# Optimization experiments

Measured on AMD Instinct MI355X. Metric: run time of the kernel, lower is better.

Reference implementation:

```python
import jax, jax.numpy as jnp
import numpy as np


def setup_inputs() -> dict:
    key = jax.random.key(0)
    ks = jax.random.split(key, 8)
    B, T, D, H, E = 4, 1024, 1024, 4096, 8
    s = 0.02
    return {
        "x": jax.random.normal(ks[0], (B, T, D), jnp.float32),
        "gate_w": jax.random.normal(ks[1], (E, D), jnp.float32) * s,
        "router_scale": jnp.ones((1,), jnp.float32),
        "w1": jax.random.normal(ks[2], (E, H, D), jnp.float32) * s,
        "b1": jnp.zeros((E, H), jnp.float32),
        "w2": jax.random.normal(ks[3], (E, H, D), jnp.float32) * s,
        "b2": jnp.zeros((E, H), jnp.float32),
        "w3": jax.random.normal(ks[4], (E, D, H), jnp.float32) * s,
        "b3": jnp.zeros((E, D), jnp.float32),
        "top_k": 2,
    }


def reference(x, gate_w, router_scale, w1, b1, w2, b2, w3, b3, top_k):
    B, T, C = x.shape
    E = gate_w.shape[0]
    xf = x.reshape(B * T, C)                     # (N, C)
    # Router: top-k over scaled gate logits, softmax over the k selected logits
    logits = (xf @ gate_w.T) * router_scale      # (N, E)
    vals, idx = jax.lax.top_k(logits, top_k)     # (N, K)
    rw = jax.nn.softmax(vals, axis=-1)           # (N, K)
    # combine[n, e] = sum_k rw[n,k] * [idx[n,k] == e]  -- per-token expert weight
    combine = jnp.sum(jax.nn.one_hot(idx, E, dtype=xf.dtype) * rw[..., None], axis=1)  # (N, E)
    y = jnp.zeros_like(xf)
    for e in range(E):  # fixed small expert count; each iter is a dense SwiGLU
        h = jax.nn.silu(xf @ w1[e].T + b1[e]) * (xf @ w2[e].T + b2[e])  # (N, H)
        out = h @ w3[e].T + b3[e]                                        # (N, C)
        y = y + out * combine[:, e:e + 1]
    return y.reshape(B, T, C)
```

## Files before the change

### kernel.cpp

```cpp
#include <hip/hip_runtime.h>
#include <hip/hip_bf16.h>

#define NTOK 4096
#define DDIM 1024
#define HDIM 4096
#define NEXP 8
#define TM 128
#define TN 128
#define BK 64
#define LDP 72

typedef __attribute__((ext_vector_type(4))) float f32x4;
typedef __attribute__((ext_vector_type(8))) short bf16x8;
typedef __attribute__((ext_vector_type(4))) short bf16x4;

static __device__ __forceinline__ short f2bf(float f) {
  union { __hip_bfloat16 b; short s; } u;
  u.b = __float2bfloat16(f);
  return u.s;
}

static __device__ __forceinline__ void gl16(const void* g, void* l) {
  __builtin_amdgcn_global_load_lds((const __attribute__((address_space(1))) void*)g,
                                   (__attribute__((address_space(3))) void*)l, 16, 0, 0);
}

__global__ __launch_bounds__(256) void router_kernel(
    const float* __restrict__ x, const float* __restrict__ gw,
    const float* __restrict__ rs,
    int* __restrict__ tok_id, float* __restrict__ tok_w,
    int* __restrict__ counts, short* __restrict__ xb)
{
  const int wv = threadIdx.x >> 6;
  const int lane = threadIdx.x & 63;
  const int tok = blockIdx.x * 4 + wv;
  const f32x4* xr = (const f32x4*)(x + (size_t)tok * DDIM);
  f32x4 xv[4];
#pragma unroll
  for (int j = 0; j < 4; ++j) xv[j] = xr[j * 64 + lane];
  if (xb) {
#pragma unroll
    for (int j = 0; j < 4; ++j) {
      bf16x4 bv = { f2bf(xv[j][0]), f2bf(xv[j][1]), f2bf(xv[j][2]), f2bf(xv[j][3]) };
      *(bf16x4*)(xb + (size_t)tok * DDIM + (size_t)(j * 64 + lane) * 4) = bv;
    }
  }
  float lg[NEXP];
#pragma unroll
  for (int e = 0; e < NEXP; ++e) {
    const f32x4* gr = (const f32x4*)(gw + (size_t)e * DDIM);
    float s = 0.f;
#pragma unroll
    for (int j = 0; j < 4; ++j) {
      f32x4 g = gr[j * 64 + lane];
      s += g[0]*xv[j][0] + g[1]*xv[j][1] + g[2]*xv[j][2] + g[3]*xv[j][3];
    }
#pragma unroll
    for (int off = 32; off > 0; off >>= 1) s += __shfl_down(s, off, 64);
    lg[e] = s;
  }
  if (lane == 0) {
    const float scale = rs[0];
#pragma unroll
    for (int e = 0; e < NEXP; ++e) lg[e] *= scale;
    int i0 = 0;
#pragma unroll
    for (int e = 1; e < NEXP; ++e) if (lg[e] > lg[i0]) i0 = e;
    int i1 = (i0 == 0) ? 1 : 0;
#pragma unroll
    for (int e = 0; e < NEXP; ++e) if (e != i0 && lg[e] > lg[i1]) i1 = e;
    const float v0 = lg[i0], v1 = lg[i1];
    const float w0 = 1.f / (1.f + expf(v1 - v0));
    const float w1v = 1.f - w0;
    int s0 = atomicAdd(&counts[i0], 1);
    tok_id[i0 * NTOK + s0] = tok;
    tok_w[i0 * NTOK + s0] = w0;
    int s1 = atomicAdd(&counts[i1], 1);
    tok_id[i1 * NTOK + s1] = tok;
    tok_w[i1 * NTOK + s1] = w1v;
  }
}

__global__ void finalize_kernel(const int* __restrict__ counts, int* __restrict__ hoff) {
  if (threadIdx.x == 0) {
    int off = 0;
    for (int e = 0; e < NEXP; ++e) { hoff[e] = off; off += ((counts[e] + TM - 1) / TM) * TM; }
  }
}

__global__ __launch_bounds__(256) void convert_kernel(
    const float* __restrict__ src, short* __restrict__ dst, int n4)
{
  int i = blockIdx.x * 256 + threadIdx.x;
  const int stride = gridDim.x * 256;
  for (; i < n4; i += stride) {
    const f32x4 v = ((const f32x4*)src)[i];
    bf16x4 b = { f2bf(v[0]), f2bf(v[1]), f2bf(v[2]), f2bf(v[3]) };
    ((bf16x4*)dst)[i] = b;
  }
}

__global__ __launch_bounds__(256, 2) void stagea_fast(
    const short* __restrict__ xb,
    const short* __restrict__ w1b, const short* __restrict__ w2b,
    const float* __restrict__ b1, const float* __restrict__ b2,
    const int* __restrict__ tok_id,
    const int* __restrict__ counts, const int* __restrict__ hoff,
    short* __restrict__ h)
{
  const int e = blockIdx.z;
  const int cnt = counts[e];
  const int mt = blockIdx.y;
  if (mt * TM >= cnt) return;
  const int nt = blockIdx.x;

  __shared__ __align__(16) short sA[TM * BK];
  __shared__ __align__(16) short sB1[TN * BK];
  __shared__ __align__(16) short sB2[TN * BK];
  __shared__ int srow[TM];

  const int t = threadIdx.x;
  const int lane = t & 63;
  const int wv = t >> 6;

  if (t < TM) {
    int id = tok_id[e * NTOK + mt * TM + t];
    srow[t] = id < 0 ? 0 : id;
  }
  __syncthreads();

  const int sub = lane >> 3;
  const int c8  = lane & 7;
  const short* wbase1 = w1b + (size_t)e * HDIM * DDIM + (size_t)(nt * TN) * DDIM;
  const short* wbase2 = w2b + (size_t)e * HDIM * DDIM + (size_t)(nt * TN) * DDIM;
  const short* ap[4]; const short* bp1[4]; const short* bp2[4];
#pragma unroll
  for (int j = 0; j < 4; ++j) {
    const int r = wv * 32 + j * 8 + sub;
    ap[j]  = xb + (size_t)srow[r] * DDIM + c8 * 8;
    bp1[j] = wbase1 + (size_t)r * DDIM + c8 * 8;
    bp2[j] = wbase2 + (size_t)r * DDIM + c8 * 8;
  }

  const int wm = (wv >> 1) * 64;
  const int wn = (wv & 1) * 64;
  const int lr = lane & 15;
  const int lq = lane >> 4;

  f32x4 acc1[4][4] = {};
  f32x4 acc2[4][4] = {};

  for (int k0 = 0; k0 < DDIM; k0 += BK) {
#pragma unroll
    for (int j = 0; j < 4; ++j) {
      gl16(ap[j] + k0,  sA  + (wv * 4 + j) * 512);
      gl16(bp1[j] + k0, sB1 + (wv * 4 + j) * 512);
      gl16(bp2[j] + k0, sB2 + (wv * 4 + j) * 512);
    }
    __syncthreads();
#pragma unroll
    for (int ks = 0; ks < BK; ks += 32) {
      bf16x8 af[4], ba[4], bb[4];
#pragma unroll
      for (int mi = 0; mi < 4; ++mi)
        af[mi] = *(const bf16x8*)(sA + (wm + mi * 16 + lr) * BK + ks + lq * 8);
#pragma unroll
      for (int ni = 0; ni < 4; ++ni) {
        ba[ni] = *(const bf16x8*)(sB1 + (wn + ni * 16 + lr) * BK + ks + lq * 8);
        bb[ni] = *(const bf16x8*)(sB2 + (wn + ni * 16 + lr) * BK + ks + lq * 8);
      }
#pragma unroll
      for (int mi = 0; mi < 4; ++mi)
#pragma unroll
        for (int ni = 0; ni < 4; ++ni) {
          acc1[mi][ni] = __builtin_amdgcn_mfma_f32_16x16x32_bf16(af[mi], ba[ni], acc1[mi][ni], 0, 0, 0);
          acc2[mi][ni] = __builtin_amdgcn_mfma_f32_16x16x32_bf16(af[mi], bb[ni], acc2[mi][ni], 0, 0, 0);
        }
    }
    __syncthreads();
  }

  const int hbase = hoff[e] + mt * TM;
#pragma unroll
  for (int ni = 0; ni < 4; ++ni) {
    const int col = nt * TN + wn + ni * 16 + lr;
    const float bb1 = b1[e * HDIM + col];
    const float bb2 = b2[e * HDIM + col];
#pragma unroll
    for (int mi = 0; mi < 4; ++mi) {
#pragma unroll
      for (int r = 0; r < 4; ++r) {
        const int row = wm + mi * 16 + lq * 4 + r;
        const float z1 = acc1[mi][ni][r] + bb1;
        const float z2 = acc2[mi][ni][r] + bb2;
        const float hv = (z1 / (1.f + expf(-z1))) * z2;
        h[(size_t)(hbase + row) * HDIM + col] = f2bf(hv);
      }
    }
  }
}

__global__ __launch_bounds__(256, 2) void stageb_fast(
    const short* __restrict__ hm, const short* __restrict__ w3b,
    const float* __restrict__ b3,
    const int* __restrict__ tok_id, const float* __restrict__ tok_w,
    const int* __restrict__ counts, const int* __restrict__ hoff,
    float* __restrict__ y)
{
  const int e = blockIdx.z;
  const int cnt = counts[e];
  const int mt = blockIdx.y;
  if (mt * TM >= cnt) return;
  const int nt = blockIdx.x & 7;
  const int kh = blockIdx.x >> 3;

  __shared__ __align__(16) short sA[TM * BK];
  __shared__ __align__(16) short sB[TN * BK];

  const int t = threadIdx.x;
  const int lane = t & 63;
  const int wv = t >> 6;
  const int sub = lane >> 3;
  const int c8  = lane & 7;

  const short* hrow = hm + (size_t)(hoff[e] + mt * TM) * HDIM;
  const short* wbase = w3b + (size_t)e * DDIM * HDIM + (size_t)(nt * TN) * HDIM;
  const short* ap[4]; const short* bp[4];
#pragma unroll
  for (int j = 0; j < 4; ++j) {
    const int r = wv * 32 + j * 8 + sub;
    ap[j] = hrow + (size_t)r * HDIM + c8 * 8;
    bp[j] = wbase + (size_t)r * HDIM + c8 * 8;
  }

  const int wm = (wv >> 1) * 64;
  const int wn = (wv & 1) * 64;
  const int lr = lane & 15;
  const int lq = lane >> 4;

  f32x4 acc[4][4] = {};

  const int kbeg = kh * (HDIM / 2);
  for (int k0 = kbeg; k0 < kbeg + HDIM / 2; k0 += BK) {
#pragma unroll
    for (int j = 0; j < 4; ++j) {
      gl16(ap[j] + k0, sA + (wv * 4 + j) * 512);
      gl16(bp[j] + k0, sB + (wv * 4 + j) * 512);
    }
    __syncthreads();
#pragma unroll
    for (int ks = 0; ks < BK; ks += 32) {
      bf16x8 af[4], bfr[4];
#pragma unroll
      for (int mi = 0; mi < 4; ++mi)
        af[mi] = *(const bf16x8*)(sA + (wm + mi * 16 + lr) * BK + ks + lq * 8);
#pragma unroll
      for (int ni = 0; ni < 4; ++ni)
        bfr[ni] = *(const bf16x8*)(sB + (wn + ni * 16 + lr) * BK + ks + lq * 8);
#pragma unroll
      for (int mi = 0; mi < 4; ++mi)
#pragma unroll
        for (int ni = 0; ni < 4; ++ni)
          acc[mi][ni] = __builtin_amdgcn_mfma_f32_16x16x32_bf16(af[mi], bfr[ni], acc[mi][ni], 0, 0, 0);
    }
    __syncthreads();
  }

#pragma unroll
  for (int ni = 0; ni < 4; ++ni) {
    const int col = nt * TN + wn + ni * 16 + lr;
    const float bb3 = (kh == 0) ? b3[e * DDIM + col] : 0.f;
#pragma unroll
    for (int mi = 0; mi < 4; ++mi) {
#pragma unroll
      for (int r = 0; r < 4; ++r) {
        const int row = mt * TM + wm + mi * 16 + lq * 4 + r;
        const int tok = tok_id[e * NTOK + row];
        if (tok >= 0) {
          const float wgt = tok_w[e * NTOK + row];
          atomicAdd(&y[(size_t)tok * DDIM + col], wgt * (acc[mi][ni][r] + bb3));
        }
      }
    }
  }
}

__global__ __launch_bounds__(256, 2) void stagea_kernel(
    const float* __restrict__ x,
    const float* __restrict__ w1, const float* __restrict__ b1,
    const float* __restrict__ w2, const float* __restrict__ b2,
    const int* __restrict__ tok_id,
    const int* __restrict__ counts, const int* __restrict__ hoff,
    short* __restrict__ h)
{
  const int e = blockIdx.z;
  const int cnt = counts[e];
  const int mt = blockIdx.y;
  if (mt * TM >= cnt) return;
  const int nt = blockIdx.x;

  __shared__ __align__(16) short sA[TM * LDP];
  __shared__ __align__(16) short sB1[TN * LDP];
  __shared__ __align__(16) short sB2[TN * LDP];
  __shared__ int srow[TM];

  const int t = threadIdx.x;
  if (t < TM) {
    int id = tok_id[e * NTOK + mt * TM + t];
    srow[t] = id < 0 ? 0 : id;
  }

  const float* wa = w1 + (size_t)e * HDIM * DDIM + (size_t)(nt * TN) * DDIM;
  const float* wb = w2 + (size_t)e * HDIM * DDIM + (size_t)(nt * TN) * DDIM;

  const int lane = t & 63;
  const int wv = t >> 6;
  const int wm = (wv >> 1) * 64;
  const int wn = (wv & 1) * 64;
  const int lr = lane & 15;
  const int lq = lane >> 4;

  f32x4 acc1[4][4] = {};
  f32x4 acc2[4][4] = {};

  const int r0 = t >> 4;
  const int c4 = t & 15;

  for (int k0 = 0; k0 < DDIM; k0 += BK) {
    __syncthreads();
#pragma unroll
    for (int j = 0; j < 8; ++j) {
      const int r = r0 + j * 16;
      const f32x4 v = *(const f32x4*)(x + (size_t)srow[r] * DDIM + k0 + c4 * 4);
      bf16x4 bv = { f2bf(v[0]), f2bf(v[1]), f2bf(v[2]), f2bf(v[3]) };
      *(bf16x4*)(sA + r * LDP + c4 * 4) = bv;
    }
#pragma unroll
    for (int j = 0; j < 8; ++j) {
      const int r = r0 + j * 16;
      const f32x4 v1 = *(const f32x4*)(wa + (size_t)r * DDIM + k0 + c4 * 4);
      bf16x4 b1v = { f2bf(v1[0]), f2bf(v1[1]), f2bf(v1[2]), f2bf(v1[3]) };
      *(bf16x4*)(sB1 + r * LDP + c4 * 4) = b1v;
      const f32x4 v2 = *(const f32x4*)(wb + (size_t)r * DDIM + k0 + c4 * 4);
      bf16x4 b2v = { f2bf(v2[0]), f2bf(v2[1]), f2bf(v2[2]), f2bf(v2[3]) };
      *(bf16x4*)(sB2 + r * LDP + c4 * 4) = b2v;
    }
    __syncthreads();
#pragma unroll
    for (int ks = 0; ks < BK; ks += 32) {
      bf16x8 af[4], bfa[4], bfb[4];
#pragma unroll
      for (int mi = 0; mi < 4; ++mi)
        af[mi] = *(const bf16x8*)(sA + (wm + mi * 16 + lr) * LDP + ks + lq * 8);
#pragma unroll
      for (int ni = 0; ni < 4; ++ni) {
        bfa[ni] = *(const bf16x8*)(sB1 + (wn + ni * 16 + lr) * LDP + ks + lq * 8);
        bfb[ni] = *(const bf16x8*)(sB2 + (wn + ni * 16 + lr) * LDP + ks + lq * 8);
      }
#pragma unroll
      for (int mi = 0; mi < 4; ++mi)
#pragma unroll
        for (int ni = 0; ni < 4; ++ni) {
          acc1[mi][ni] = __builtin_amdgcn_mfma_f32_16x16x32_bf16(af[mi], bfa[ni], acc1[mi][ni], 0, 0, 0);
          acc2[mi][ni] = __builtin_amdgcn_mfma_f32_16x16x32_bf16(af[mi], bfb[ni], acc2[mi][ni], 0, 0, 0);
        }
    }
  }

  const int hbase = hoff[e] + mt * TM;
#pragma unroll
  for (int ni = 0; ni < 4; ++ni) {
    const int col = nt * TN + wn + ni * 16 + lr;
    const float bb1 = b1[e * HDIM + col];
    const float bb2 = b2[e * HDIM + col];
#pragma unroll
    for (int mi = 0; mi < 4; ++mi) {
#pragma unroll
      for (int r = 0; r < 4; ++r) {
        const int row = wm + mi * 16 + lq * 4 + r;
        const float z1 = acc1[mi][ni][r] + bb1;
        const float z2 = acc2[mi][ni][r] + bb2;
        const float hv = (z1 / (1.f + expf(-z1))) * z2;
        h[(size_t)(hbase + row) * HDIM + col] = f2bf(hv);
      }
    }
  }
}

__global__ __launch_bounds__(256, 2) void stageb_kernel(
    const short* __restrict__ h,
    const float* __restrict__ w3, const float* __restrict__ b3,
    const int* __restrict__ tok_id, const float* __restrict__ tok_w,
    const int* __restrict__ counts, const int* __restrict__ hoff,
    float* __restrict__ y)
{
  const int e = blockIdx.z;
  const int cnt = counts[e];
  const int mt = blockIdx.y;
  if (mt * TM >= cnt) return;
  const int nt = blockIdx.x;

  __shared__ __align__(16) short sA[TM * LDP];
  __shared__ __align__(16) short sB[TN * LDP];

  const int t = threadIdx.x;
  const int lane = t & 63;
  const int wv = t >> 6;
  const int wm = (wv >> 1) * 64;
  const int wn = (wv & 1) * 64;
  const int lr = lane & 15;
  const int lq = lane >> 4;

  const short* hrow = h + (size_t)(hoff[e] + mt * TM) * HDIM;
  const float* wc = w3 + (size_t)e * DDIM * HDIM + (size_t)(nt * TN) * HDIM;

  f32x4 acc[4][4] = {};

  const int rA = t >> 3;
  const int c8 = t & 7;
  const int rB = t >> 4;
  const int c4 = t & 15;

  for (int k0 = 0; k0 < HDIM; k0 += BK) {
    __syncthreads();
#pragma unroll
    for (int j = 0; j < 4; ++j) {
      const int r = rA + j * 32;
      bf16x8 v = *(const bf16x8*)(hrow + (size_t)r * HDIM + k0 + c8 * 8);
      *(bf16x8*)(sA + r * LDP + c8 * 8) = v;
    }
#pragma unroll
    for (int j = 0; j < 8; ++j) {
      const int r = rB + j * 16;
      const f32x4 v = *(const f32x4*)(wc + (size_t)r * HDIM + k0 + c4 * 4);
      bf16x4 bv = { f2bf(v[0]), f2bf(v[1]), f2bf(v[2]), f2bf(v[3]) };
      *(bf16x4*)(sB + r * LDP + c4 * 4) = bv;
    }
    __syncthreads();
#pragma unroll
    for (int ks = 0; ks < BK; ks += 32) {
      bf16x8 af[4], bfr[4];
#pragma unroll
      for (int mi = 0; mi < 4; ++mi)
        af[mi] = *(const bf16x8*)(sA + (wm + mi * 16 + lr) * LDP + ks + lq * 8);
#pragma unroll
      for (int ni = 0; ni < 4; ++ni)
        bfr[ni] = *(const bf16x8*)(sB + (wn + ni * 16 + lr) * LDP + ks + lq * 8);
#pragma unroll
      for (int mi = 0; mi < 4; ++mi)
#pragma unroll
        for (int ni = 0; ni < 4; ++ni)
          acc[mi][ni] = __builtin_amdgcn_mfma_f32_16x16x32_bf16(af[mi], bfr[ni], acc[mi][ni], 0, 0, 0);
    }
  }

#pragma unroll
  for (int ni = 0; ni < 4; ++ni) {
    const int col = nt * TN + wn + ni * 16 + lr;
    const float bb3 = b3[e * DDIM + col];
#pragma unroll
    for (int mi = 0; mi < 4; ++mi) {
#pragma unroll
      for (int r = 0; r < 4; ++r) {
        const int row = mt * TM + wm + mi * 16 + lq * 4 + r;
        const int tok = tok_id[e * NTOK + row];
        if (tok >= 0) {
          const float wgt = tok_w[e * NTOK + row];
          atomicAdd(&y[(size_t)tok * DDIM + col], wgt * (acc[mi][ni][r] + bb3));
        }
      }
    }
  }
}

extern "C" void kernel_launch(void* const* d_in, const int* in_sizes, int n_in,
                              void* d_out, int out_size, void* d_ws, size_t ws_size,
                              hipStream_t stream) {
  const float* x  = (const float*)d_in[0];
  const float* gw = (const float*)d_in[1];
  const float* rs = (const float*)d_in[2];
  const float* w1 = (const float*)d_in[3];
  const float* b1 = (const float*)d_in[4];
  const float* w2 = (const float*)d_in[5];
  const float* b2 = (const float*)d_in[6];
  const float* w3 = (const float*)d_in[7];
  const float* b3 = (const float*)d_in[8];

  char* ws = (char*)d_ws;
  int*   tok_id = (int*)ws;
  float* tok_w  = (float*)(ws + 131072);
  int*   counts = (int*)(ws + 262144);
  int*   hoff   = (int*)(ws + 262176);

  const size_t OFF_XB = 262656;
  const size_t OFF_H  = OFF_XB + 8388608ull;
  const size_t OFF_WB = OFF_H  + 75497472ull;
  const size_t FAST_REQ = OFF_WB + 134217728ull;
  const bool fast = ws_size >= FAST_REQ;

  hipMemsetAsync(counts, 0, 32, stream);
  hipMemsetAsync(tok_id, 0xFF, 131072, stream);
  hipMemsetAsync(d_out, 0, (size_t)out_size * sizeof(float), stream);

  if (fast) {
    short* xb  = (short*)(ws + OFF_XB);
    short* h   = (short*)(ws + OFF_H);
    short* w1b = (short*)(ws + OFF_WB);
    short* w2b = w1b + 33554432;
    const int W4 = 8388608;

    router_kernel<<<dim3(NTOK / 4), dim3(256), 0, stream>>>(x, gw, rs, tok_id, tok_w, counts, xb);
    finalize_kernel<<<dim3(1), dim3(64), 0, stream>>>(counts, hoff);
    convert_kernel<<<dim3(2048), dim3(256), 0, stream>>>(w1, w1b, W4);
    convert_kernel<<<dim3(2048), dim3(256), 0, stream>>>(w2, w2b, W4);
    stagea_fast<<<dim3(HDIM / TN, NTOK / TM, NEXP), dim3(256), 0, stream>>>(
        xb, w1b, w2b, b1, b2, tok_id, counts, hoff, h);
    convert_kernel<<<dim3(2048), dim3(256), 0, stream>>>(w3, w1b, W4);
    stageb_fast<<<dim3(2 * (DDIM / TN), NTOK / TM, NEXP), dim3(256), 0, stream>>>(
        h, w1b, b3, tok_id, tok_w, counts, hoff, (float*)d_out);
  } else {
    short* h = (short*)(ws + 262656);
    router_kernel<<<dim3(NTOK / 4), dim3(256), 0, stream>>>(x, gw, rs, tok_id, tok_w, counts, (short*)nullptr);
    finalize_kernel<<<dim3(1), dim3(64), 0, stream>>>(counts, hoff);
    stagea_kernel<<<dim3(HDIM / TN, NTOK / TM, NEXP), dim3(256), 0, stream>>>(
        x, w1, b1, w2, b2, tok_id, counts, hoff, h);
    stageb_kernel<<<dim3(DDIM / TN, NTOK / TM, NEXP), dim3(256), 0, stream>>>(
        h, w3, b3, tok_id, tok_w, counts, hoff, (float*)d_out);
  }
}
```

Baseline: 911.9 us.

## Swizzle LDS tiles and replace atomic scatter with partial buffer plus gather

XOR-swizzles the shared-memory column layout in both expert GEMMs, so MFMA fragment reads avoid LDS bank conflicts. Stage B drops its split-K and float atomicAdd scatter. Each routed slot now writes its weighted row to a partial buffer. A new gather kernel sums each token's two slot rows into the output, which also removes the output memset on the fast path. The cost is an extra kernel and extra global traffic for the partial buffer, plus fewer stage-B blocks.

Result: faster. 825.3 us (-9.5%).

```diff
diff --git a/kernel.cpp b/kernel.cpp
--- a/kernel.cpp
+++ b/kernel.cpp
@@ -29,7 +29,7 @@
     const float* __restrict__ x, const float* __restrict__ gw,
     const float* __restrict__ rs,
     int* __restrict__ tok_id, float* __restrict__ tok_w,
-    int* __restrict__ counts, short* __restrict__ xb)
+    int* __restrict__ counts, short* __restrict__ xb, int* __restrict__ tok_slot)
 {
   const int wv = threadIdx.x >> 6;
   const int lane = threadIdx.x & 63;
@@ -78,6 +78,8 @@
     int s1 = atomicAdd(&counts[i1], 1);
     tok_id[i1 * NTOK + s1] = tok;
     tok_w[i1 * NTOK + s1] = w1v;
+    tok_slot[tok * 2 + 0] = i0 * NTOK + s0;
+    tok_slot[tok * 2 + 1] = i1 * NTOK + s1;
   }
 }
 
@@ -131,21 +133,25 @@
 
   const int sub = lane >> 3;
   const int c8  = lane & 7;
+  const int csw = (c8 ^ sub) * 8;
   const short* wbase1 = w1b + (size_t)e * HDIM * DDIM + (size_t)(nt * TN) * DDIM;
   const short* wbase2 = w2b + (size_t)e * HDIM * DDIM + (size_t)(nt * TN) * DDIM;
   const short* ap[4]; const short* bp1[4]; const short* bp2[4];
 #pragma unroll
   for (int j = 0; j < 4; ++j) {
     const int r = wv * 32 + j * 8 + sub;
-    ap[j]  = xb + (size_t)srow[r] * DDIM + c8 * 8;
-    bp1[j] = wbase1 + (size_t)r * DDIM + c8 * 8;
-    bp2[j] = wbase2 + (size_t)r * DDIM + c8 * 8;
+    ap[j]  = xb + (size_t)srow[r] * DDIM + csw;
+    bp1[j] = wbase1 + (size_t)r * DDIM + csw;
+    bp2[j] = wbase2 + (size_t)r * DDIM + csw;
   }
 
   const int wm = (wv >> 1) * 64;
   const int wn = (wv & 1) * 64;
   const int lr = lane & 15;
   const int lq = lane >> 4;
+  const int r7 = lr & 7;
+  const int sw0 = ((lq ^ r7) << 3);
+  const int sw1 = (((4 + lq) ^ r7) << 3);
 
   f32x4 acc1[4][4] = {};
   f32x4 acc2[4][4] = {};
@@ -159,15 +165,16 @@
     }
     __syncthreads();
 #pragma unroll
-    for (int ks = 0; ks < BK; ks += 32) {
+    for (int ks = 0; ks < 2; ++ks) {
+      const int sw = ks ? sw1 : sw0;
       bf16x8 af[4], ba[4], bb[4];
 #pragma unroll
       for (int mi = 0; mi < 4; ++mi)
-        af[mi] = *(const bf16x8*)(sA + (wm + mi * 16 + lr) * BK + ks + lq * 8);
+        af[mi] = *(const bf16x8*)(sA + (wm + mi * 16 + lr) * BK + sw);
 #pragma unroll
       for (int ni = 0; ni < 4; ++ni) {
-        ba[ni] = *(const bf16x8*)(sB1 + (wn + ni * 16 + lr) * BK + ks + lq * 8);
-        bb[ni] = *(const bf16x8*)(sB2 + (wn + ni * 16 + lr) * BK + ks + lq * 8);
+        ba[ni] = *(const bf16x8*)(sB1 + (wn + ni * 16 + lr) * BK + sw);
+        bb[ni] = *(const bf16x8*)(sB2 + (wn + ni * 16 + lr) * BK + sw);
       }
 #pragma unroll
       for (int mi = 0; mi < 4; ++mi)
@@ -202,17 +209,15 @@
 
 __global__ __launch_bounds__(256, 2) void stageb_fast(
     const short* __restrict__ hm, const short* __restrict__ w3b,
-    const float* __restrict__ b3,
-    const int* __restrict__ tok_id, const float* __restrict__ tok_w,
+    const float* __restrict__ b3, const float* __restrict__ tok_w,
     const int* __restrict__ counts, const int* __restrict__ hoff,
-    float* __restrict__ y)
+    float* __restrict__ pout)
 {
   const int e = blockIdx.z;
   const int cnt = counts[e];
   const int mt = blockIdx.y;
   if (mt * TM >= cnt) return;
-  const int nt = blockIdx.x & 7;
-  const int kh = blockIdx.x >> 3;
+  const int nt = blockIdx.x;
 
   __shared__ __align__(16) short sA[TM * BK];
   __shared__ __align__(16) short sB[TN * BK];
@@ -222,6 +227,7 @@
   const int wv = t >> 6;
   const int sub = lane >> 3;
   const int c8  = lane & 7;
+  const int csw = (c8 ^ sub) * 8;
 
   const short* hrow = hm + (size_t)(hoff[e] + mt * TM) * HDIM;
   const short* wbase = w3b + (size_t)e * DDIM * HDIM + (size_t)(nt * TN) * HDIM;
@@ -229,19 +235,21 @@
 #pragma unroll
   for (int j = 0; j < 4; ++j) {
     const int r = wv * 32 + j * 8 + sub;
-    ap[j] = hrow + (size_t)r * HDIM + c8 * 8;
-    bp[j] = wbase + (size_t)r * HDIM + c8 * 8;
+    ap[j] = hrow + (size_t)r * HDIM + csw;
+    bp[j] = wbase + (size_t)r * HDIM + csw;
   }
 
   const int wm = (wv >> 1) * 64;
   const int wn = (wv & 1) * 64;
   const int lr = lane & 15;
   const int lq = lane >> 4;
+  const int r7 = lr & 7;
+  const int sw0 = ((lq ^ r7) << 3);
+  const int sw1 = (((4 + lq) ^ r7) << 3);
 
   f32x4 acc[4][4] = {};
 
-  const int kbeg = kh * (HDIM / 2);
-  for (int k0 = kbeg; k0 < kbeg + HDIM / 2; k0 += BK) {
+  for (int k0 = 0; k0 < HDIM; k0 += BK) {
 #pragma unroll
     for (int j = 0; j < 4; ++j) {
       gl16(ap[j] + k0, sA + (wv * 4 + j) * 512);
@@ -249,14 +257,15 @@
     }
     __syncthreads();
 #pragma unroll
-    for (int ks = 0; ks < BK; ks += 32) {
+    for (int ks = 0; ks < 2; ++ks) {
+      const int sw = ks ? sw1 : sw0;
       bf16x8 af[4], bfr[4];
 #pragma unroll
       for (int mi = 0; mi < 4; ++mi)
-        af[mi] = *(const bf16x8*)(sA + (wm + mi * 16 + lr) * BK + ks + lq * 8);
+        af[mi] = *(const bf16x8*)(sA + (wm + mi * 16 + lr) * BK + sw);
 #pragma unroll
       for (int ni = 0; ni < 4; ++ni)
-        bfr[ni] = *(const bf16x8*)(sB + (wn + ni * 16 + lr) * BK + ks + lq * 8);
+        bfr[ni] = *(const bf16x8*)(sB + (wn + ni * 16 + lr) * BK + sw);
 #pragma unroll
       for (int mi = 0; mi < 4; ++mi)
 #pragma unroll
@@ -266,23 +275,36 @@
     __syncthreads();
   }
 
+  float* prow = pout + (size_t)(hoff[e] + mt * TM) * DDIM;
 #pragma unroll
   for (int ni = 0; ni < 4; ++ni) {
     const int col = nt * TN + wn + ni * 16 + lr;
-    const float bb3 = (kh == 0) ? b3[e * DDIM + col] : 0.f;
+    const float bb3 = b3[e * DDIM + col];
 #pragma unroll
     for (int mi = 0; mi < 4; ++mi) {
 #pragma unroll
       for (int r = 0; r < 4; ++r) {
-        const int row = mt * TM + wm + mi * 16 + lq * 4 + r;
-        const int tok = tok_id[e * NTOK + row];
-        if (tok >= 0) {
-          const float wgt = tok_w[e * NTOK + row];
-          atomicAdd(&y[(size_t)tok * DDIM + col], wgt * (acc[mi][ni][r] + bb3));
-        }
+        const int row = wm + mi * 16 + lq * 4 + r;
+        const float wgt = tok_w[e * NTOK + mt * TM + row];
+        prow[(size_t)row * DDIM + col] = wgt * (acc[mi][ni][r] + bb3);
       }
     }
   }
+}
+
+__global__ __launch_bounds__(256) void gather_kernel(
+    const float* __restrict__ pout, const int* __restrict__ tok_slot,
+    const int* __restrict__ hoff, float* __restrict__ y)
+{
+  const int tok = blockIdx.x;
+  const int c = threadIdx.x;
+  const int es0 = tok_slot[tok * 2 + 0];
+  const int es1 = tok_slot[tok * 2 + 1];
+  const size_t p0 = (size_t)(hoff[es0 >> 12] + (es0 & 4095));
+  const size_t p1 = (size_t)(hoff[es1 >> 12] + (es1 & 4095));
+  const f32x4 a = ((const f32x4*)pout)[p0 * 256 + c];
+  const f32x4 b = ((const f32x4*)pout)[p1 * 256 + c];
+  ((f32x4*)y)[(size_t)tok * 256 + c] = a + b;
 }
 
 __global__ __launch_bounds__(256, 2) void stagea_kernel(
@@ -487,12 +509,13 @@
   const float* b3 = (const float*)d_in[8];
 
   char* ws = (char*)d_ws;
-  int*   tok_id = (int*)ws;
-  float* tok_w  = (float*)(ws + 131072);
-  int*   counts = (int*)(ws + 262144);
-  int*   hoff   = (int*)(ws + 262176);
-
-  const size_t OFF_XB = 262656;
+  int*   tok_id   = (int*)ws;
+  float* tok_w    = (float*)(ws + 131072);
+  int*   counts   = (int*)(ws + 262144);
+  int*   hoff     = (int*)(ws + 262176);
+  int*   tok_slot = (int*)(ws + 262208);
+
+  const size_t OFF_XB = 295168;
   const size_t OFF_H  = OFF_XB + 8388608ull;
   const size_t OFF_WB = OFF_H  + 75497472ull;
   const size_t FAST_REQ = OFF_WB + 134217728ull;
@@ -500,27 +523,29 @@
 
   hipMemsetAsync(counts, 0, 32, stream);
   hipMemsetAsync(tok_id, 0xFF, 131072, stream);
-  hipMemsetAsync(d_out, 0, (size_t)out_size * sizeof(float), stream);
 
   if (fast) {
-    short* xb  = (short*)(ws + OFF_XB);
-    short* h   = (short*)(ws + OFF_H);
-    short* w1b = (short*)(ws + OFF_WB);
-    short* w2b = w1b + 33554432;
+    short* xb   = (short*)(ws + OFF_XB);
+    short* h    = (short*)(ws + OFF_H);
+    short* w1b  = (short*)(ws + OFF_WB);
+    short* w2b  = w1b + 33554432;
+    float* pout = (float*)(ws + OFF_WB + 67108864ull);
     const int W4 = 8388608;
 
-    router_kernel<<<dim3(NTOK / 4), dim3(256), 0, stream>>>(x, gw, rs, tok_id, tok_w, counts, xb);
+    router_kernel<<<dim3(NTOK / 4), dim3(256), 0, stream>>>(x, gw, rs, tok_id, tok_w, counts, xb, tok_slot);
     finalize_kernel<<<dim3(1), dim3(64), 0, stream>>>(counts, hoff);
     convert_kernel<<<dim3(2048), dim3(256), 0, stream>>>(w1, w1b, W4);
     convert_kernel<<<dim3(2048), dim3(256), 0, stream>>>(w2, w2b, W4);
     stagea_fast<<<dim3(HDIM / TN, NTOK / TM, NEXP), dim3(256), 0, stream>>>(
         xb, w1b, w2b, b1, b2, tok_id, counts, hoff, h);
     convert_kernel<<<dim3(2048), dim3(256), 0, stream>>>(w3, w1b, W4);
-    stageb_fast<<<dim3(2 * (DDIM / TN), NTOK / TM, NEXP), dim3(256), 0, stream>>>(
-        h, w1b, b3, tok_id, tok_w, counts, hoff, (float*)d_out);
+    stageb_fast<<<dim3(DDIM / TN, NTOK / TM, NEXP), dim3(256), 0, stream>>>(
+        h, w1b, b3, tok_w, counts, hoff, pout);
+    gather_kernel<<<dim3(NTOK), dim3(256), 0, stream>>>(pout, tok_slot, hoff, (float*)d_out);
   } else {
-    short* h = (short*)(ws + 262656);
-    router_kernel<<<dim3(NTOK / 4), dim3(256), 0, stream>>>(x, gw, rs, tok_id, tok_w, counts, (short*)nullptr);
+    short* h = (short*)(ws + OFF_XB);
+    hipMemsetAsync(d_out, 0, (size_t)out_size * sizeof(float), stream);
+    router_kernel<<<dim3(NTOK / 4), dim3(256), 0, stream>>>(x, gw, rs, tok_id, tok_w, counts, (short*)nullptr, tok_slot);
     finalize_kernel<<<dim3(1), dim3(64), 0, stream>>>(counts, hoff);
     stagea_kernel<<<dim3(HDIM / TN, NTOK / TM, NEXP), dim3(256), 0, stream>>>(
         x, w1, b1, w2, b2, tok_id, counts, hoff, h);
```
